# Performance work log

Measured on AMD Instinct MI355X. Metric: run time of the kernel, lower is better.

Reference implementation:

```python
import jax, jax.numpy as jnp
import numpy as np

E, I, H, T = 8, 2816, 1024, 8192

def setup_inputs() -> dict:
    key = jax.random.key(0)
    ks = jax.random.split(key, 5)
    scale_w = 1.0 / np.sqrt(H)
    return {
        "hidden_states": jax.random.normal(ks[0], (T, H), jnp.float32),
        "router_logits": jax.random.normal(ks[1], (T, E), jnp.float32),
        "W1": jax.random.normal(ks[2], (E, I, H), jnp.float32) * scale_w,
        "W3": jax.random.normal(ks[3], (E, I, H), jnp.float32) * scale_w,
        "W2": jax.random.normal(ks[4], (E, H, I), jnp.float32) * (1.0 / np.sqrt(I)),
        "top_k": 2,
    }

def reference(hidden_states, router_logits, W1, W3, W2, top_k):
    # softmax router in fp32, topk, renormalize (renormalize=True, use_grouped_topk=False)
    probs = jax.nn.softmax(router_logits.astype(jnp.float32), axis=-1)  # [T,E]
    vals, idx = jax.lax.top_k(probs, top_k)                             # [T,K]
    vals = vals / jnp.sum(vals, axis=-1, keepdims=True)
    vals = vals.astype(hidden_states.dtype)
    n_tok, n_exp = probs.shape
    # dense per-token expert weight matrix [T,E]; zero for unrouted experts,
    # mathematically identical to the gather/scatter-add in the ipex op
    w = jnp.zeros((n_tok, n_exp), hidden_states.dtype).at[
        jnp.arange(n_tok)[:, None], idx].add(vals)

    def expert_step(acc, args):
        We1, We3, We2, we = args  # [I,H], [I,H], [H,I], [T]
        h = jax.nn.silu(hidden_states @ We1.T) * (hidden_states @ We3.T)  # [T,I]
        return acc + we[:, None] * (h @ We2.T), None

    out, _ = jax.lax.scan(expert_step, jnp.zeros_like(hidden_states),
                          (W1, W3, W2, w.T))
    return out
```

## Files before the change

### kernel.cpp

```cpp
#include <hip/hip_runtime.h>
#include <stdint.h>

#define NE 8
#define NI 2816
#define NH 1024
#define NT 8192
#define NPAIR (NT * 2)

typedef __bf16 bf16x8 __attribute__((ext_vector_type(8)));
typedef float f32x4 __attribute__((ext_vector_type(4)));

__device__ __forceinline__ uint16_t f2bf(float f) {
    union { float f; uint32_t u; } v;
    v.f = f;
    return (uint16_t)((v.u + 0x7FFFu + ((v.u >> 16) & 1u)) >> 16);
}

__device__ __forceinline__ float bflo(uint32_t u) {
    union { uint32_t x; float f; } v; v.x = u << 16; return v.f;
}
__device__ __forceinline__ float bfhi(uint32_t u) {
    union { uint32_t x; float f; } v; v.x = u & 0xffff0000u; return v.f;
}

__device__ __forceinline__ void gld16(const void* g, void* l) {
    __builtin_amdgcn_global_load_lds(
        (__attribute__((address_space(1))) void*)(uintptr_t)g,
        (__attribute__((address_space(3))) void*)(uint32_t)(uintptr_t)l,
        16, 0, 0);
}

__global__ __launch_bounds__(256) void k_cvt3(const float* __restrict__ W1,
                                              const float* __restrict__ W3,
                                              const float* __restrict__ W2,
                                              uint16_t* __restrict__ W1b,
                                              uint16_t* __restrict__ W3b,
                                              uint16_t* __restrict__ W2b) {
    int i = blockIdx.x * 256 + threadIdx.x;
    const float* s = blockIdx.y == 0 ? W1 : (blockIdx.y == 1 ? W3 : W2);
    uint16_t* d = blockIdx.y == 0 ? W1b : (blockIdx.y == 1 ? W3b : W2b);
    float4 a = ((const float4*)s)[(size_t)i * 2];
    float4 b = ((const float4*)s)[(size_t)i * 2 + 1];
    uint4 o;
    o.x = (uint32_t)f2bf(a.x) | ((uint32_t)f2bf(a.y) << 16);
    o.y = (uint32_t)f2bf(a.z) | ((uint32_t)f2bf(a.w) << 16);
    o.z = (uint32_t)f2bf(b.x) | ((uint32_t)f2bf(b.y) << 16);
    o.w = (uint32_t)f2bf(b.z) | ((uint32_t)f2bf(b.w) << 16);
    ((uint4*)d)[i] = o;
}

__global__ __launch_bounds__(256) void k_router(const float* __restrict__ logits,
                                                int* __restrict__ tok_e,
                                                float2* __restrict__ tok_w,
                                                int* __restrict__ counts) {
    int t = blockIdx.x * 256 + threadIdx.x;
    if (t >= NT) return;
    float4 a = ((const float4*)logits)[(size_t)t * 2];
    float4 b = ((const float4*)logits)[(size_t)t * 2 + 1];
    float l[8] = {a.x, a.y, a.z, a.w, b.x, b.y, b.z, b.w};
    int i0 = 0; float l0 = l[0];
#pragma unroll
    for (int e = 1; e < 8; e++) if (l[e] > l0) { l0 = l[e]; i0 = e; }
    int i1 = -1; float l1 = -3.4e38f;
#pragma unroll
    for (int e = 0; e < 8; e++) if (e != i0 && l[e] > l1) { l1 = l[e]; i1 = e; }
    float w0 = 1.f / (1.f + __expf(l1 - l0));
    float w1 = 1.f - w0;
    tok_e[t] = i0 | (i1 << 8);
    tok_w[t] = make_float2(w0, w1);
    atomicAdd(&counts[i0], 1);
    atomicAdd(&counts[i1], 1);
}

__global__ void k_scan(const int* __restrict__ counts, int* __restrict__ offsets,
                       int* __restrict__ cursor) {
    if (threadIdx.x == 0) {
        int o = 0;
        for (int e = 0; e < NE; e++) { offsets[e] = o; cursor[e] = o; o += counts[e]; }
    }
}

__global__ __launch_bounds__(128) void k_gather(const float* __restrict__ x,
                                                const int* __restrict__ tok_e,
                                                const float2* __restrict__ tok_w,
                                                int* __restrict__ cursor,
                                                uint16_t* __restrict__ Xg,
                                                int2* __restrict__ tok_slots,
                                                float* __restrict__ slot_w) {
    int t = blockIdx.x;
    __shared__ int ss[2];
    if (threadIdx.x == 0) {
        int ee = tok_e[t];
        float2 w = tok_w[t];
        int s0 = atomicAdd(&cursor[ee & 0xff], 1);
        int s1 = atomicAdd(&cursor[(ee >> 8) & 0xff], 1);
        ss[0] = s0; ss[1] = s1;
        tok_slots[t] = make_int2(s0, s1);
        slot_w[s0] = w.x;
        slot_w[s1] = w.y;
    }
    __syncthreads();
    int s0 = ss[0], s1 = ss[1];
    int i = threadIdx.x;
    const float4* xr = (const float4*)(x + (size_t)t * NH);
    float4 a = xr[i * 2];
    float4 b = xr[i * 2 + 1];
    uint4 o;
    o.x = (uint32_t)f2bf(a.x) | ((uint32_t)f2bf(a.y) << 16);
    o.y = (uint32_t)f2bf(a.z) | ((uint32_t)f2bf(a.w) << 16);
    o.z = (uint32_t)f2bf(b.x) | ((uint32_t)f2bf(b.y) << 16);
    o.w = (uint32_t)f2bf(b.z) | ((uint32_t)f2bf(b.w) << 16);
    ((uint4*)(Xg + (size_t)s0 * NH))[i] = o;
    ((uint4*)(Xg + (size_t)s1 * NH))[i] = o;
}

__global__ __launch_bounds__(256, 2) void k_gemm1(const uint16_t* __restrict__ Xg,
                                                  const uint16_t* __restrict__ W1b,
                                                  const uint16_t* __restrict__ W3b,
                                                  uint16_t* __restrict__ Hbuf,
                                                  const int* __restrict__ counts,
                                                  const int* __restrict__ offsets) {
    int e = blockIdx.z;
    int n_e = counts[e];
    int mtile = blockIdx.y;
    if (mtile * 128 >= n_e) return;
    int ntile = blockIdx.x;
    int off = offsets[e];

    __shared__ __align__(16) uint16_t As[128 * 32];
    __shared__ __align__(16) uint16_t B1s[128 * 32];
    __shared__ __align__(16) uint16_t B3s[128 * 32];

    int tid = threadIdx.x;
    int r = tid >> 2, c = tid & 3;
    int wv = tid >> 6, lane = tid & 63;
    int wr = wv >> 1, wc = wv & 1;
    int m_in = lane & 15, q = lane >> 4;

    int rowA0 = off + mtile * 128 + r;
    int rowA1 = min(rowA0 + 64, NPAIR - 1);
    rowA0 = min(rowA0, NPAIR - 1);
    const uint16_t* a0 = Xg + (size_t)rowA0 * NH + c * 8;
    const uint16_t* a1 = Xg + (size_t)rowA1 * NH + c * 8;
    const uint16_t* b1r = W1b + ((size_t)e * NI + ntile * 128 + r) * NH + c * 8;
    const uint16_t* b3r = W3b + ((size_t)e * NI + ntile * 128 + r) * NH + c * 8;

    uint16_t* lA0 = &As[tid * 8];   uint16_t* lA1 = &As[2048 + tid * 8];
    uint16_t* lB10 = &B1s[tid * 8]; uint16_t* lB11 = &B1s[2048 + tid * 8];
    uint16_t* lB30 = &B3s[tid * 8]; uint16_t* lB31 = &B3s[2048 + tid * 8];

    const uint16_t* pa = &As[(wr * 64 + m_in) * 32 + q * 8];
    const uint16_t* pb1 = &B1s[(wc * 64 + m_in) * 32 + q * 8];
    const uint16_t* pb3 = &B3s[(wc * 64 + m_in) * 32 + q * 8];

    f32x4 acc1[4][4] = {};
    f32x4 acc3[4][4] = {};

    for (int k0 = 0; k0 < NH; k0 += 32) {
        gld16(a0 + k0, lA0);
        gld16(a1 + k0, lA1);
        gld16(b1r + k0, lB10);
        gld16(b1r + (size_t)64 * NH + k0, lB11);
        gld16(b3r + k0, lB30);
        gld16(b3r + (size_t)64 * NH + k0, lB31);
        __syncthreads();

        bf16x8 af[4], b1f[4], b3f[4];
#pragma unroll
        for (int it = 0; it < 4; it++) af[it] = *(const bf16x8*)(pa + it * 512);
#pragma unroll
        for (int jt = 0; jt < 4; jt++) {
            b1f[jt] = *(const bf16x8*)(pb1 + jt * 512);
            b3f[jt] = *(const bf16x8*)(pb3 + jt * 512);
        }
#pragma unroll
        for (int it = 0; it < 4; it++)
#pragma unroll
            for (int jt = 0; jt < 4; jt++) {
                acc1[it][jt] = __builtin_amdgcn_mfma_f32_16x16x32_bf16(af[it], b1f[jt], acc1[it][jt], 0, 0, 0);
                acc3[it][jt] = __builtin_amdgcn_mfma_f32_16x16x32_bf16(af[it], b3f[jt], acc3[it][jt], 0, 0, 0);
            }
        __syncthreads();
    }

    int sBase = off + mtile * 128;
#pragma unroll
    for (int it = 0; it < 4; it++) {
#pragma unroll
        for (int reg = 0; reg < 4; reg++) {
            int lm = wr * 64 + it * 16 + q * 4 + reg;
            if (mtile * 128 + lm < n_e) {
                uint16_t* orow = Hbuf + (size_t)(sBase + lm) * NI + ntile * 128 + wc * 64 + m_in;
#pragma unroll
                for (int jt = 0; jt < 4; jt++) {
                    float c1 = acc1[it][jt][reg];
                    float c3 = acc3[it][jt][reg];
                    float hv = (c1 / (1.f + __expf(-c1))) * c3;
                    orow[jt * 16] = f2bf(hv);
                }
            }
        }
    }
}

__global__ __launch_bounds__(256, 2) void k_gemm2(const uint16_t* __restrict__ Hbuf,
                                                  const uint16_t* __restrict__ W2b,
                                                  uint16_t* __restrict__ Ybuf,
                                                  const int* __restrict__ counts,
                                                  const int* __restrict__ offsets) {
    int e = blockIdx.z;
    int n_e = counts[e];
    int mtile = blockIdx.y;
    if (mtile * 128 >= n_e) return;
    int ntile = blockIdx.x;
    int off = offsets[e];

    __shared__ __align__(16) uint16_t As[128 * 32];
    __shared__ __align__(16) uint16_t Bs[128 * 32];

    int tid = threadIdx.x;
    int r = tid >> 2, c = tid & 3;
    int wv = tid >> 6, lane = tid & 63;
    int wr = wv >> 1, wc = wv & 1;
    int m_in = lane & 15, q = lane >> 4;

    int rowA0 = off + mtile * 128 + r;
    int rowA1 = min(rowA0 + 64, NPAIR - 1);
    rowA0 = min(rowA0, NPAIR - 1);
    const uint16_t* a0 = Hbuf + (size_t)rowA0 * NI + c * 8;
    const uint16_t* a1 = Hbuf + (size_t)rowA1 * NI + c * 8;
    const uint16_t* br = W2b + ((size_t)e * NH + ntile * 128 + r) * NI + c * 8;

    uint16_t* lA0 = &As[tid * 8]; uint16_t* lA1 = &As[2048 + tid * 8];
    uint16_t* lB0 = &Bs[tid * 8]; uint16_t* lB1 = &Bs[2048 + tid * 8];

    const uint16_t* pa = &As[(wr * 64 + m_in) * 32 + q * 8];
    const uint16_t* pb = &Bs[(wc * 64 + m_in) * 32 + q * 8];

    f32x4 acc[4][4] = {};

    for (int k0 = 0; k0 < NI; k0 += 32) {
        gld16(a0 + k0, lA0);
        gld16(a1 + k0, lA1);
        gld16(br + k0, lB0);
        gld16(br + (size_t)64 * NI + k0, lB1);
        __syncthreads();

        bf16x8 af[4], bf[4];
#pragma unroll
        for (int it = 0; it < 4; it++) af[it] = *(const bf16x8*)(pa + it * 512);
#pragma unroll
        for (int jt = 0; jt < 4; jt++) bf[jt] = *(const bf16x8*)(pb + jt * 512);
#pragma unroll
        for (int it = 0; it < 4; it++)
#pragma unroll
            for (int jt = 0; jt < 4; jt++)
                acc[it][jt] = __builtin_amdgcn_mfma_f32_16x16x32_bf16(af[it], bf[jt], acc[it][jt], 0, 0, 0);
        __syncthreads();
    }

    int sBase = off + mtile * 128;
#pragma unroll
    for (int it = 0; it < 4; it++) {
#pragma unroll
        for (int reg = 0; reg < 4; reg++) {
            int lm = wr * 64 + it * 16 + q * 4 + reg;
            if (mtile * 128 + lm < n_e) {
                uint16_t* orow = Ybuf + (size_t)(sBase + lm) * NH + ntile * 128 + wc * 64 + m_in;
#pragma unroll
                for (int jt = 0; jt < 4; jt++)
                    orow[jt * 16] = f2bf(acc[it][jt][reg]);
            }
        }
    }
}

__global__ __launch_bounds__(256) void k_combine(const uint16_t* __restrict__ Y,
                                                 const int2* __restrict__ tok_slots,
                                                 const float* __restrict__ slot_w,
                                                 float* __restrict__ out) {
    int idx = blockIdx.x * 256 + threadIdx.x;
    int t = idx >> 7;
    int g = idx & 127;
    int2 s = tok_slots[t];
    float w0 = slot_w[s.x], w1 = slot_w[s.y];
    uint4 u0 = ((const uint4*)(Y + (size_t)s.x * NH))[g];
    uint4 u1 = ((const uint4*)(Y + (size_t)s.y * NH))[g];
    float4 o0, o1;
    o0.x = w0 * bflo(u0.x) + w1 * bflo(u1.x);
    o0.y = w0 * bfhi(u0.x) + w1 * bfhi(u1.x);
    o0.z = w0 * bflo(u0.y) + w1 * bflo(u1.y);
    o0.w = w0 * bfhi(u0.y) + w1 * bfhi(u1.y);
    o1.x = w0 * bflo(u0.z) + w1 * bflo(u1.z);
    o1.y = w0 * bfhi(u0.z) + w1 * bfhi(u1.z);
    o1.z = w0 * bflo(u0.w) + w1 * bflo(u1.w);
    o1.w = w0 * bfhi(u0.w) + w1 * bfhi(u1.w);
    float4* orow = (float4*)(out + (size_t)t * NH + g * 8);
    orow[0] = o0;
    orow[1] = o1;
}

extern "C" void kernel_launch(void* const* d_in, const int* in_sizes, int n_in,
                              void* d_out, int out_size, void* d_ws, size_t ws_size,
                              hipStream_t stream) {
    const float* x = (const float*)d_in[0];
    const float* logits = (const float*)d_in[1];
    const float* W1 = (const float*)d_in[2];
    const float* W3 = (const float*)d_in[3];
    const float* W2 = (const float*)d_in[4];
    float* out = (float*)d_out;

    char* ws = (char*)d_ws;
    size_t o = 0;
    auto nxt = [&](size_t b) -> void* {
        void* p = ws + o;
        o += (b + 255) & ~(size_t)255;
        return p;
    };
    const size_t WELEMS = (size_t)NE * NI * NH;
    uint16_t* W1b = (uint16_t*)nxt(WELEMS * 2);
    uint16_t* W3b = (uint16_t*)nxt(WELEMS * 2);
    uint16_t* W2b = (uint16_t*)nxt(WELEMS * 2);
    uint16_t* Xg = (uint16_t*)nxt((size_t)NPAIR * NH * 2);
    uint16_t* Hbuf = (uint16_t*)nxt((size_t)NPAIR * NI * 2);
    float* slot_w = (float*)nxt((size_t)NPAIR * 4);
    int2* tok_slots = (int2*)nxt((size_t)NT * 8);
    int* tok_e = (int*)nxt((size_t)NT * 4);
    float2* tok_w = (float2*)nxt((size_t)NT * 8);
    int* meta = (int*)nxt(128);
    int* counts = meta;
    int* offsets = meta + 8;
    int* cursor = meta + 16;
    uint16_t* Ybuf = Xg;
    (void)ws_size; (void)in_sizes; (void)n_in;

    hipMemsetAsync(meta, 0, 128, stream);

    k_router<<<NT / 256, 256, 0, stream>>>(logits, tok_e, tok_w, counts);
    k_scan<<<1, 64, 0, stream>>>(counts, offsets, cursor);

    k_cvt3<<<dim3((unsigned)(WELEMS / 8 / 256), 3), 256, 0, stream>>>(W1, W3, W2, W1b, W3b, W2b);

    k_gather<<<NT, 128, 0, stream>>>(x, tok_e, tok_w, cursor, Xg, tok_slots, slot_w);

    k_gemm1<<<dim3(NI / 128, NT / 128, NE), 256, 0, stream>>>(Xg, W1b, W3b, Hbuf, counts, offsets);
    k_gemm2<<<dim3(NH / 128, NT / 128, NE), 256, 0, stream>>>(Hbuf, W2b, Ybuf, counts, offsets);
    k_combine<<<NT * NH / 8 / 256, 256, 0, stream>>>(Ybuf, tok_slots, slot_w, out);
}
```

Before: 961.5 us.

## Replace MoE GEMMs with 256x256 pipelined 8-wave kernel and interleaved W1/W3

Interleaves W1 and W3 rows in 16-row groups during bf16 conversion so the gate/up GEMM becomes a single GEMM over 2*NI columns. Both grouped GEMMs now use one templated 512-thread kernel with 256x256 tiles, K-step 64, double-buffered 128KB LDS fed by global_load_lds, XOR-swizzled LDS layout, and a hand-scheduled phase loop with explicit barriers, waitcnts and setprio. The aim is to raise MFMA utilization and data reuse and to hide global load latency behind compute. The larger tiles waste more work on partially filled per-expert M tiles, and the large LDS footprint limits occupancy.

```diff
diff --git a/kernel.cpp b/kernel.cpp
--- a/kernel.cpp
+++ b/kernel.cpp
@@ -30,23 +30,37 @@
         16, 0, 0);
 }
 
-__global__ __launch_bounds__(256) void k_cvt3(const float* __restrict__ W1,
-                                              const float* __restrict__ W3,
-                                              const float* __restrict__ W2,
-                                              uint16_t* __restrict__ W1b,
-                                              uint16_t* __restrict__ W3b,
-                                              uint16_t* __restrict__ W2b) {
-    int i = blockIdx.x * 256 + threadIdx.x;
-    const float* s = blockIdx.y == 0 ? W1 : (blockIdx.y == 1 ? W3 : W2);
-    uint16_t* d = blockIdx.y == 0 ? W1b : (blockIdx.y == 1 ? W3b : W2b);
-    float4 a = ((const float4*)s)[(size_t)i * 2];
-    float4 b = ((const float4*)s)[(size_t)i * 2 + 1];
+__global__ __launch_bounds__(256) void k_cvt_w13(const float* __restrict__ W1,
+                                                 const float* __restrict__ W3,
+                                                 uint16_t* __restrict__ Wg) {
+    int row = blockIdx.x * 2 + (threadIdx.x >> 7);
+    int g = threadIdx.x & 127;
+    const float* src = (blockIdx.y == 0) ? W1 : W3;
+    int e = row / NI;
+    int r = row - e * NI;
+    size_t drow = (size_t)e * (2 * NI) + (size_t)((r >> 4) * 32 + (r & 15) + (blockIdx.y ? 16 : 0));
+    const float4* sp = (const float4*)(src + (size_t)row * NH);
+    float4 a = sp[g * 2];
+    float4 b = sp[g * 2 + 1];
     uint4 o;
     o.x = (uint32_t)f2bf(a.x) | ((uint32_t)f2bf(a.y) << 16);
     o.y = (uint32_t)f2bf(a.z) | ((uint32_t)f2bf(a.w) << 16);
     o.z = (uint32_t)f2bf(b.x) | ((uint32_t)f2bf(b.y) << 16);
     o.w = (uint32_t)f2bf(b.z) | ((uint32_t)f2bf(b.w) << 16);
-    ((uint4*)d)[i] = o;
+    ((uint4*)(Wg + drow * NH))[g] = o;
+}
+
+__global__ __launch_bounds__(256) void k_cvt_flat(const float* __restrict__ S,
+                                                  uint16_t* __restrict__ D) {
+    size_t i = (size_t)blockIdx.x * 256 + threadIdx.x;
+    float4 a = ((const float4*)S)[i * 2];
+    float4 b = ((const float4*)S)[i * 2 + 1];
+    uint4 o;
+    o.x = (uint32_t)f2bf(a.x) | ((uint32_t)f2bf(a.y) << 16);
+    o.y = (uint32_t)f2bf(a.z) | ((uint32_t)f2bf(a.w) << 16);
+    o.z = (uint32_t)f2bf(b.x) | ((uint32_t)f2bf(b.y) << 16);
+    o.w = (uint32_t)f2bf(b.z) | ((uint32_t)f2bf(b.w) << 16);
+    ((uint4*)D)[i] = o;
 }
 
 __global__ __launch_bounds__(256) void k_router(const float* __restrict__ logits,
@@ -114,162 +128,180 @@
     ((uint4*)(Xg + (size_t)s1 * NH))[i] = o;
 }
 
-__global__ __launch_bounds__(256, 2) void k_gemm1(const uint16_t* __restrict__ Xg,
-                                                  const uint16_t* __restrict__ W1b,
-                                                  const uint16_t* __restrict__ W3b,
-                                                  uint16_t* __restrict__ Hbuf,
-                                                  const int* __restrict__ counts,
-                                                  const int* __restrict__ offsets) {
+
+#define BAR()  asm volatile("s_barrier" ::: "memory")
+#define WAITLGKM asm volatile("s_waitcnt lgkmcnt(0)" ::: "memory")
+#define WAITV4 asm volatile("s_waitcnt vmcnt(4)" ::: "memory")
+#define WAITV0 asm volatile("s_waitcnt vmcnt(0)" ::: "memory")
+#define SCHB __builtin_amdgcn_sched_barrier(0)
+#define PRIO1 __builtin_amdgcn_s_setprio(1)
+#define PRIO0 __builtin_amdgcn_s_setprio(0)
+
+#define STAGE(ab, bufsel, h, kt)                                                  \
+    do {                                                                          \
+        char* d_ = lds + (bufsel) * 65536 + (ab) * 32768 + (h) * 16384 + tid * 16; \
+        gld16(((ab) ? srcB : srcA)[h][0] + (kt) * 64, d_);                         \
+        gld16(((ab) ? srcB : srcA)[h][1] + (kt) * 64, d_ + 8192);                  \
+    } while (0)
+
+#define READA(bufsel, mh)                                                           \
+    do {                                                                            \
+        _Pragma("unroll") for (int ii = 0; ii < 4; ii++) {                          \
+            const char* p_ = lds + (bufsel) * 65536 + wr * 16384 +                  \
+                             (((mh) * 4 + ii) * 16 + l15) * 128;                    \
+            af[ii][0] = *(const bf16x8*)(p_ + colk0);                               \
+            af[ii][1] = *(const bf16x8*)(p_ + colk1);                               \
+        }                                                                           \
+    } while (0)
+
+#define READB(bufsel, nh, dst)                                                      \
+    do {                                                                            \
+        _Pragma("unroll") for (int jj = 0; jj < 2; jj++) {                          \
+            int gb_ = wc * 64 + ((nh) * 2 + jj) * 16;                               \
+            const char* p_ = lds + (bufsel) * 65536 + 32768 + (gb_ >> 7) * 16384 +  \
+                             ((gb_ & 127) + l15) * 128;                             \
+            dst[jj][0] = *(const bf16x8*)(p_ + colk0);                              \
+            dst[jj][1] = *(const bf16x8*)(p_ + colk1);                              \
+        }                                                                           \
+    } while (0)
+
+#define MMQ(mh, bsrc, jb)                                                           \
+    do {                                                                            \
+        _Pragma("unroll") for (int ii = 0; ii < 4; ii++)                            \
+            _Pragma("unroll") for (int jj = 0; jj < 2; jj++)                        \
+                _Pragma("unroll") for (int ks = 0; ks < 2; ks++)                    \
+                    acc[(mh) * 4 + ii][(jb) + jj] =                                 \
+                        __builtin_amdgcn_mfma_f32_16x16x32_bf16(                    \
+                            af[ii][ks], bsrc[jj][ks], acc[(mh) * 4 + ii][(jb) + jj],\
+                            0, 0, 0);                                               \
+    } while (0)
+
+#define PHASES(i2, LAST)                                                            \
+    do {                                                                            \
+        int t1_ = (i2) + 1, t2_ = (i2) + 2, t3_ = (i2) + 3;                         \
+                                                                            \
+        READA(0, 0); READB(0, 0, b0);                                               \
+        STAGE(0, 1, 0, t1_); STAGE(0, 1, 1, t1_);                                   \
+        BAR(); WAITLGKM; SCHB; PRIO1; MMQ(0, b0, 0); PRIO0; SCHB; BAR();            \
+                                                                            \
+        READB(0, 1, b1);                                                            \
+        BAR(); WAITLGKM; SCHB; PRIO1; MMQ(0, b1, 2); PRIO0; SCHB; BAR();            \
+                                                                            \
+        READA(0, 1);                                                                \
+        if (!(LAST)) STAGE(1, 0, 0, t2_);                                           \
+        BAR(); WAITLGKM; SCHB; PRIO1; MMQ(1, b1, 2); PRIO0; SCHB; BAR();            \
+                                                                            \
+        if (!(LAST)) STAGE(1, 0, 1, t2_);                                           \
+        BAR(); PRIO1; MMQ(1, b0, 0); PRIO0; SCHB;                                   \
+        if (LAST) { WAITV0; } else { WAITV4; }                                      \
+        BAR();                                                                      \
+                                                                            \
+        READA(1, 0); READB(1, 0, b0);                                               \
+        if (!(LAST)) { STAGE(0, 0, 0, t2_); STAGE(0, 0, 1, t2_); }                  \
+        BAR(); WAITLGKM; SCHB; PRIO1; MMQ(0, b0, 0); PRIO0; SCHB; BAR();            \
+                                                                            \
+        READB(1, 1, b1);                                                            \
+        BAR(); WAITLGKM; SCHB; PRIO1; MMQ(0, b1, 2); PRIO0; SCHB; BAR();            \
+                                                                            \
+        READA(1, 1);                                                                \
+        if (!(LAST)) STAGE(1, 1, 0, t3_);                                           \
+        BAR(); WAITLGKM; SCHB; PRIO1; MMQ(1, b1, 2); PRIO0; SCHB; BAR();            \
+                                                                            \
+        if (!(LAST)) STAGE(1, 1, 1, t3_);                                           \
+        BAR(); PRIO1; MMQ(1, b0, 0); PRIO0; SCHB;                                   \
+        if (LAST) { WAITV0; } else { WAITV4; }                                      \
+        BAR();                                                                      \
+    } while (0)
+
+template <int MODE>
+__global__ __launch_bounds__(512, 2) void k_moe_gemm(const uint16_t* __restrict__ Abase,
+                                                     const uint16_t* __restrict__ Bbase,
+                                                     uint16_t* __restrict__ Cbase,
+                                                     const int* __restrict__ counts,
+                                                     const int* __restrict__ offsets) {
+    constexpr int K = (MODE == 1) ? NH : NI;
+    constexpr int NKT = K / 64;
+    constexpr int NITER = NKT / 2;
+    constexpr int BROWS = (MODE == 1) ? 2 * NI : NH;
+    constexpr int CLD = (MODE == 1) ? NI : NH;
+
     int e = blockIdx.z;
     int n_e = counts[e];
     int mtile = blockIdx.y;
-    if (mtile * 128 >= n_e) return;
+    if (mtile * 256 >= n_e) return;
     int ntile = blockIdx.x;
     int off = offsets[e];
 
-    __shared__ __align__(16) uint16_t As[128 * 32];
-    __shared__ __align__(16) uint16_t B1s[128 * 32];
-    __shared__ __align__(16) uint16_t B3s[128 * 32];
+    __shared__ __align__(16) char lds[131072];
 
     int tid = threadIdx.x;
-    int r = tid >> 2, c = tid & 3;
-    int wv = tid >> 6, lane = tid & 63;
-    int wr = wv >> 1, wc = wv & 1;
-    int m_in = lane & 15, q = lane >> 4;
-
-    int rowA0 = off + mtile * 128 + r;
-    int rowA1 = min(rowA0 + 64, NPAIR - 1);
-    rowA0 = min(rowA0, NPAIR - 1);
-    const uint16_t* a0 = Xg + (size_t)rowA0 * NH + c * 8;
-    const uint16_t* a1 = Xg + (size_t)rowA1 * NH + c * 8;
-    const uint16_t* b1r = W1b + ((size_t)e * NI + ntile * 128 + r) * NH + c * 8;
-    const uint16_t* b3r = W3b + ((size_t)e * NI + ntile * 128 + r) * NH + c * 8;
-
-    uint16_t* lA0 = &As[tid * 8];   uint16_t* lA1 = &As[2048 + tid * 8];
-    uint16_t* lB10 = &B1s[tid * 8]; uint16_t* lB11 = &B1s[2048 + tid * 8];
-    uint16_t* lB30 = &B3s[tid * 8]; uint16_t* lB31 = &B3s[2048 + tid * 8];
-
-    const uint16_t* pa = &As[(wr * 64 + m_in) * 32 + q * 8];
-    const uint16_t* pb1 = &B1s[(wc * 64 + m_in) * 32 + q * 8];
-    const uint16_t* pb3 = &B3s[(wc * 64 + m_in) * 32 + q * 8];
-
-    f32x4 acc1[4][4] = {};
-    f32x4 acc3[4][4] = {};
-
-    for (int k0 = 0; k0 < NH; k0 += 32) {
-        gld16(a0 + k0, lA0);
-        gld16(a1 + k0, lA1);
-        gld16(b1r + k0, lB10);
-        gld16(b1r + (size_t)64 * NH + k0, lB11);
-        gld16(b3r + k0, lB30);
-        gld16(b3r + (size_t)64 * NH + k0, lB31);
-        __syncthreads();
-
-        bf16x8 af[4], b1f[4], b3f[4];
-#pragma unroll
-        for (int it = 0; it < 4; it++) af[it] = *(const bf16x8*)(pa + it * 512);
-#pragma unroll
-        for (int jt = 0; jt < 4; jt++) {
-            b1f[jt] = *(const bf16x8*)(pb1 + jt * 512);
-            b3f[jt] = *(const bf16x8*)(pb3 + jt * 512);
+    int l15 = tid & 15;
+    int q = (tid >> 4) & 3;
+    int x7 = tid & 7;
+    int wv = tid >> 6, wr = wv >> 2, wc = wv & 3;
+    int colk0 = (q ^ x7) << 4;
+    int colk1 = ((q + 4) ^ x7) << 4;
+
+    int sr = tid >> 3;
+    int ss = x7 ^ (sr & 7);
+    const uint16_t* srcA[2][2];
+    const uint16_t* srcB[2][2];
+#pragma unroll
+    for (int h = 0; h < 2; h++)
+#pragma unroll
+        for (int j = 0; j < 2; j++) {
+            int gr = off + mtile * 256 + h * 128 + j * 64 + sr;
+            gr = min(gr, NPAIR - 1);
+            srcA[h][j] = Abase + (size_t)gr * K + ss * 8;
+            int gn = ntile * 256 + h * 128 + j * 64 + sr;
+            srcB[h][j] = Bbase + (size_t)e * BROWS * K + (size_t)gn * K + ss * 8;
         }
-#pragma unroll
-        for (int it = 0; it < 4; it++)
-#pragma unroll
-            for (int jt = 0; jt < 4; jt++) {
-                acc1[it][jt] = __builtin_amdgcn_mfma_f32_16x16x32_bf16(af[it], b1f[jt], acc1[it][jt], 0, 0, 0);
-                acc3[it][jt] = __builtin_amdgcn_mfma_f32_16x16x32_bf16(af[it], b3f[jt], acc3[it][jt], 0, 0, 0);
-            }
-        __syncthreads();
-    }
-
-    int sBase = off + mtile * 128;
-#pragma unroll
-    for (int it = 0; it < 4; it++) {
-#pragma unroll
-        for (int reg = 0; reg < 4; reg++) {
-            int lm = wr * 64 + it * 16 + q * 4 + reg;
-            if (mtile * 128 + lm < n_e) {
-                uint16_t* orow = Hbuf + (size_t)(sBase + lm) * NI + ntile * 128 + wc * 64 + m_in;
-#pragma unroll
-                for (int jt = 0; jt < 4; jt++) {
-                    float c1 = acc1[it][jt][reg];
-                    float c3 = acc3[it][jt][reg];
-                    float hv = (c1 / (1.f + __expf(-c1))) * c3;
-                    orow[jt * 16] = f2bf(hv);
+
+    bf16x8 af[4][2], b0[2][2], b1[2][2];
+    f32x4 acc[8][4] = {};
+
+    STAGE(0, 0, 0, 0); STAGE(0, 0, 1, 0);
+    STAGE(1, 0, 0, 0); STAGE(1, 0, 1, 0);
+    STAGE(1, 1, 0, 1); STAGE(1, 1, 1, 1);
+    WAITV4;
+    BAR();
+
+#pragma unroll 1
+    for (int it2 = 0; it2 < NITER - 1; it2++) { PHASES(2 * it2, 0); }
+    PHASES(2 * (NITER - 1), 1);
+
+    int sBase = off + mtile * 256;
+    if constexpr (MODE == 1) {
+#pragma unroll
+        for (int im = 0; im < 8; im++) {
+#pragma unroll
+            for (int r = 0; r < 4; r++) {
+                int lm = wr * 128 + im * 16 + q * 4 + r;
+                if (mtile * 256 + lm < n_e) {
+                    uint16_t* orow = Cbase + (size_t)(sBase + lm) * CLD +
+                                     ntile * 128 + wc * 32 + l15;
+#pragma unroll
+                    for (int j = 0; j < 2; j++) {
+                        float c1 = acc[im][2 * j][r];
+                        float c3 = acc[im][2 * j + 1][r];
+                        float hv = (c1 / (1.f + __expf(-c1))) * c3;
+                        orow[j * 16] = f2bf(hv);
+                    }
                 }
             }
         }
-    }
-}
-
-__global__ __launch_bounds__(256, 2) void k_gemm2(const uint16_t* __restrict__ Hbuf,
-                                                  const uint16_t* __restrict__ W2b,
-                                                  uint16_t* __restrict__ Ybuf,
-                                                  const int* __restrict__ counts,
-                                                  const int* __restrict__ offsets) {
-    int e = blockIdx.z;
-    int n_e = counts[e];
-    int mtile = blockIdx.y;
-    if (mtile * 128 >= n_e) return;
-    int ntile = blockIdx.x;
-    int off = offsets[e];
-
-    __shared__ __align__(16) uint16_t As[128 * 32];
-    __shared__ __align__(16) uint16_t Bs[128 * 32];
-
-    int tid = threadIdx.x;
-    int r = tid >> 2, c = tid & 3;
-    int wv = tid >> 6, lane = tid & 63;
-    int wr = wv >> 1, wc = wv & 1;
-    int m_in = lane & 15, q = lane >> 4;
-
-    int rowA0 = off + mtile * 128 + r;
-    int rowA1 = min(rowA0 + 64, NPAIR - 1);
-    rowA0 = min(rowA0, NPAIR - 1);
-    const uint16_t* a0 = Hbuf + (size_t)rowA0 * NI + c * 8;
-    const uint16_t* a1 = Hbuf + (size_t)rowA1 * NI + c * 8;
-    const uint16_t* br = W2b + ((size_t)e * NH + ntile * 128 + r) * NI + c * 8;
-
-    uint16_t* lA0 = &As[tid * 8]; uint16_t* lA1 = &As[2048 + tid * 8];
-    uint16_t* lB0 = &Bs[tid * 8]; uint16_t* lB1 = &Bs[2048 + tid * 8];
-
-    const uint16_t* pa = &As[(wr * 64 + m_in) * 32 + q * 8];
-    const uint16_t* pb = &Bs[(wc * 64 + m_in) * 32 + q * 8];
-
-    f32x4 acc[4][4] = {};
-
-    for (int k0 = 0; k0 < NI; k0 += 32) {
-        gld16(a0 + k0, lA0);
-        gld16(a1 + k0, lA1);
-        gld16(br + k0, lB0);
-        gld16(br + (size_t)64 * NI + k0, lB1);
-        __syncthreads();
-
-        bf16x8 af[4], bf[4];
-#pragma unroll
-        for (int it = 0; it < 4; it++) af[it] = *(const bf16x8*)(pa + it * 512);
-#pragma unroll
-        for (int jt = 0; jt < 4; jt++) bf[jt] = *(const bf16x8*)(pb + jt * 512);
-#pragma unroll
-        for (int it = 0; it < 4; it++)
-#pragma unroll
-            for (int jt = 0; jt < 4; jt++)
-                acc[it][jt] = __builtin_amdgcn_mfma_f32_16x16x32_bf16(af[it], bf[jt], acc[it][jt], 0, 0, 0);
-        __syncthreads();
-    }
-
-    int sBase = off + mtile * 128;
-#pragma unroll
-    for (int it = 0; it < 4; it++) {
-#pragma unroll
-        for (int reg = 0; reg < 4; reg++) {
-            int lm = wr * 64 + it * 16 + q * 4 + reg;
-            if (mtile * 128 + lm < n_e) {
-                uint16_t* orow = Ybuf + (size_t)(sBase + lm) * NH + ntile * 128 + wc * 64 + m_in;
-#pragma unroll
-                for (int jt = 0; jt < 4; jt++)
-                    orow[jt * 16] = f2bf(acc[it][jt][reg]);
+    } else {
+#pragma unroll
+        for (int im = 0; im < 8; im++) {
+#pragma unroll
+            for (int r = 0; r < 4; r++) {
+                int lm = wr * 128 + im * 16 + q * 4 + r;
+                if (mtile * 256 + lm < n_e) {
+                    uint16_t* orow = Cbase + (size_t)(sBase + lm) * CLD +
+                                     ntile * 256 + wc * 64 + l15;
+#pragma unroll
+                    for (int jn = 0; jn < 4; jn++) orow[jn * 16] = f2bf(acc[im][jn][r]);
+                }
             }
         }
     }
@@ -318,8 +350,7 @@
         return p;
     };
     const size_t WELEMS = (size_t)NE * NI * NH;
-    uint16_t* W1b = (uint16_t*)nxt(WELEMS * 2);
-    uint16_t* W3b = (uint16_t*)nxt(WELEMS * 2);
+    uint16_t* Wg = (uint16_t*)nxt(WELEMS * 2 * 2);
     uint16_t* W2b = (uint16_t*)nxt(WELEMS * 2);
     uint16_t* Xg = (uint16_t*)nxt((size_t)NPAIR * NH * 2);
     uint16_t* Hbuf = (uint16_t*)nxt((size_t)NPAIR * NI * 2);
@@ -339,11 +370,15 @@
     k_router<<<NT / 256, 256, 0, stream>>>(logits, tok_e, tok_w, counts);
     k_scan<<<1, 64, 0, stream>>>(counts, offsets, cursor);
 
-    k_cvt3<<<dim3((unsigned)(WELEMS / 8 / 256), 3), 256, 0, stream>>>(W1, W3, W2, W1b, W3b, W2b);
+    k_cvt_w13<<<dim3(NE * NI / 2, 2), 256, 0, stream>>>(W1, W3, Wg);
+    k_cvt_flat<<<(unsigned)(WELEMS / 8 / 256), 256, 0, stream>>>(W2, W2b);
 
     k_gather<<<NT, 128, 0, stream>>>(x, tok_e, tok_w, cursor, Xg, tok_slots, slot_w);
 
-    k_gemm1<<<dim3(NI / 128, NT / 128, NE), 256, 0, stream>>>(Xg, W1b, W3b, Hbuf, counts, offsets);
-    k_gemm2<<<dim3(NH / 128, NT / 128, NE), 256, 0, stream>>>(Hbuf, W2b, Ybuf, counts, offsets);
+    k_moe_gemm<1><<<dim3(2 * NI / 256, NT / 256, NE), 512, 0, stream>>>(
+        Xg, Wg, Hbuf, counts, offsets);
+    k_moe_gemm<2><<<dim3(NH / 256, NT / 256, NE), 512, 0, stream>>>(
+        Hbuf, W2b, Ybuf, counts, offsets);
+
     k_combine<<<NT * NH / 8 / 256, 256, 0, stream>>>(Ybuf, tok_slots, slot_w, out);
 }
```

Measured after the change: 907.2 us. -5.6%, faster.
